# Performance work log

Hardware: AMD Instinct MI355X
Metric: run time of the kernel (lower is better)

The kernel has to match this reference:

```python
import jax, jax.numpy as jnp
import numpy as np

B, L, S, D, H, TOPK = 8, 2048, 1000, 1024, 8, 10
E = D // H  # d_keys = 128


def setup_inputs() -> dict:
    key = jax.random.key(0)
    ks = jax.random.split(key, 8)
    s = 1.0 / np.sqrt(D)
    return {
        "target_embedding": jax.random.normal(ks[0], (B, L, D), dtype=jnp.float32),
        "source_embedding": jax.random.normal(ks[1], (S, D), dtype=jnp.float32),
        "Wq": jax.random.normal(ks[2], (D, D), dtype=jnp.float32) * s,
        "bq": jnp.zeros((D,), dtype=jnp.float32),
        "Wk": jax.random.normal(ks[3], (D, D), dtype=jnp.float32) * s,
        "bk": jnp.zeros((D,), dtype=jnp.float32),
        "Wo": jax.random.normal(ks[4], (D, D), dtype=jnp.float32) * s,
        "bo": jnp.zeros((D,), dtype=jnp.float32),
        "data_id": 0,
    }


def reference(target_embedding, source_embedding, Wq, bq, Wk, bk, Wo, bo, data_id):
    # data_id is unused by the original module's math.
    b, l, d = target_embedding.shape
    h, e, topk = H, E, TOPK
    scale = 1.0 / np.sqrt(e)

    q = (target_embedding @ Wq + bq).reshape(b, l, h, e)   # [B,L,H,E]
    k = (source_embedding @ Wk + bk).reshape(-1, h, e)      # [S,H,E]

    scores = jnp.einsum('blhe,she->bhls', q, k)             # [B,H,L,S]
    A = jax.nn.softmax(scale * scores, axis=-1)             # dropout is eval-mode identity
    tmps = A.sum(axis=2)                                    # [B,H,S] head-wise column mass
    _, idxs = jax.lax.top_k(tmps, topk)                     # [B,H,topk]

    kh = jnp.transpose(k, (1, 0, 2))                        # [H,S,E]
    # gather per (batch, head) the topk source key vectors
    tok = kh[jnp.arange(h)[None, :, None], idxs, :]         # [B,H,topk,E]
    tok = jnp.transpose(tok, (0, 2, 1, 3)).reshape(b, topk, h * e)  # [B,topk,D]
    return tok @ Wo + bo                                    # [B,topk,D]
```

## Files before the change

kernel.cpp:

```cpp
#include <hip/hip_runtime.h>
#include <hip/hip_bf16.h>
#include <math.h>

constexpr int B_ = 8;
constexpr int L_ = 2048;
constexpr int S_ = 1000;
constexpr int D_ = 1024;
constexpr int H_ = 8;
constexpr int E_ = 128;
constexpr int TOPK_ = 10;
constexpr float SCALE_LOG2E_ = 0.12751744f;

typedef __attribute__((ext_vector_type(8))) short short8;
typedef __attribute__((ext_vector_type(4))) float f32x4;

__device__ inline unsigned short f2bf(float x) {
    unsigned u = __float_as_uint(x);
    unsigned r = (u + 0x7fffu + ((u >> 16) & 1u)) >> 16;
    return (unsigned short)r;
}
__device__ inline float bf2f(unsigned short s) {
    return __uint_as_float(((unsigned)s) << 16);
}

__device__ __forceinline__ float fexp2(float x) {
#if __has_builtin(__builtin_amdgcn_exp2f)
    return __builtin_amdgcn_exp2f(x);
#else
    return __expf(x * 0.69314718056f);
#endif
}

typedef __attribute__((address_space(1))) const unsigned int gas_u32;
typedef __attribute__((address_space(3))) unsigned int las_u32;
__device__ __forceinline__ void gload_lds16(const void* g, void* l) {
    __builtin_amdgcn_global_load_lds((gas_u32*)g, (las_u32*)l, 16, 0, 0);
}

__global__ __launch_bounds__(256) void gemm_bias_kernel(
    const float* __restrict__ A, const float* __restrict__ Bm,
    const float* __restrict__ bias, float* __restrict__ C,
    int M, int N, int Kd)
{
    __shared__ float As[16][65];
    __shared__ float Bs[16][68];

    const int t  = threadIdx.x;
    const int tx = t & 15;
    const int ty = t >> 4;
    const int m0 = blockIdx.y * 64;
    const int n0 = blockIdx.x * 64;

    float acc[4][4];
#pragma unroll
    for (int i = 0; i < 4; ++i)
#pragma unroll
        for (int j = 0; j < 4; ++j) acc[i][j] = 0.f;

    for (int k0 = 0; k0 < Kd; k0 += 16) {
        {
            const int row = t >> 2;
            const int c4  = (t & 3) * 4;
            float4 v = {0.f, 0.f, 0.f, 0.f};
            if (m0 + row < M)
                v = *(const float4*)&A[(size_t)(m0 + row) * Kd + k0 + c4];
            As[c4 + 0][row] = v.x;
            As[c4 + 1][row] = v.y;
            As[c4 + 2][row] = v.z;
            As[c4 + 3][row] = v.w;
        }
        {
            const int row = t >> 4;
            const int c4  = (t & 15) * 4;
            float4 v = *(const float4*)&Bm[(size_t)(k0 + row) * N + n0 + c4];
            *(float4*)&Bs[row][c4] = v;
        }
        __syncthreads();
#pragma unroll
        for (int k = 0; k < 16; ++k) {
            float a[4], b[4];
#pragma unroll
            for (int i = 0; i < 4; ++i) a[i] = As[k][ty * 4 + i];
            float4 bv = *(const float4*)&Bs[k][tx * 4];
            b[0] = bv.x; b[1] = bv.y; b[2] = bv.z; b[3] = bv.w;
#pragma unroll
            for (int i = 0; i < 4; ++i)
#pragma unroll
                for (int j = 0; j < 4; ++j) acc[i][j] += a[i] * b[j];
        }
        __syncthreads();
    }

#pragma unroll
    for (int i = 0; i < 4; ++i) {
        const int row = m0 + ty * 4 + i;
        if (row < M) {
#pragma unroll
            for (int j = 0; j < 4; ++j) {
                const int col = n0 + tx * 4 + j;
                C[(size_t)row * N + col] = acc[i][j] + bias[col];
            }
        }
    }
}

__global__ __launch_bounds__(256) void splitWT_kernel(
    const float* __restrict__ W,
    unsigned short* __restrict__ WTh, unsigned short* __restrict__ WTl)
{
    __shared__ __attribute__((aligned(16))) float tile[64][68];
    const int t  = threadIdx.x;
    const int k0 = blockIdx.y * 64, n0 = blockIdx.x * 64;
#pragma unroll
    for (int it = 0; it < 4; ++it) {
        int id = it * 256 + t;
        int r = id >> 4, c = id & 15;
        *(float4*)&tile[r][c * 4] = *(const float4*)&W[(size_t)(k0 + r) * D_ + n0 + c * 4];
    }
    __syncthreads();
#pragma unroll
    for (int it = 0; it < 4; ++it) {
        int id = it * 256 + t;
        int n = id >> 4, c = id & 15;
        unsigned short hs[4], ls[4];
#pragma unroll
        for (int i = 0; i < 4; ++i) {
            float x = tile[c * 4 + i][n];
            hs[i] = f2bf(x);
            ls[i] = f2bf(x - bf2f(hs[i]));
        }
        size_t o = (size_t)(n0 + n) * D_ + k0 + c * 4;
        uint2 uh; uh.x = (unsigned)hs[0] | ((unsigned)hs[1] << 16);
                  uh.y = (unsigned)hs[2] | ((unsigned)hs[3] << 16);
        uint2 ul; ul.x = (unsigned)ls[0] | ((unsigned)ls[1] << 16);
                  ul.y = (unsigned)ls[2] | ((unsigned)ls[3] << 16);
        *(uint2*)&WTh[o] = uh;
        *(uint2*)&WTl[o] = ul;
    }
}

__global__ __launch_bounds__(256) void split_src_kernel(
    const float* __restrict__ src,
    unsigned short* __restrict__ Sh, unsigned short* __restrict__ Sl)
{
    int idx  = blockIdx.x * 256 + threadIdx.x;
    int base = idx * 4;
    int row  = base >> 10;
    float4 v = {0.f, 0.f, 0.f, 0.f};
    if (row < S_) v = *(const float4*)&src[base];
    float xs[4] = {v.x, v.y, v.z, v.w};
    unsigned short hs[4], ls[4];
#pragma unroll
    for (int i = 0; i < 4; ++i) {
        hs[i] = f2bf(xs[i]);
        ls[i] = f2bf(xs[i] - bf2f(hs[i]));
    }
    uint2 uh; uh.x = (unsigned)hs[0] | ((unsigned)hs[1] << 16);
              uh.y = (unsigned)hs[2] | ((unsigned)hs[3] << 16);
    uint2 ul; ul.x = (unsigned)ls[0] | ((unsigned)ls[1] << 16);
              ul.y = (unsigned)ls[2] | ((unsigned)ls[3] << 16);
    *(uint2*)&Sh[base] = uh;
    *(uint2*)&Sl[base] = ul;
}

__global__ __launch_bounds__(256, 2) void kproj_kernel(
    const unsigned short* __restrict__ Sh, const unsigned short* __restrict__ Sl,
    const unsigned short* __restrict__ WkTh, const unsigned short* __restrict__ WkTl,
    const float* __restrict__ bk,
    float* __restrict__ Kbuf,
    unsigned short* __restrict__ Kh, unsigned short* __restrict__ Kl)
{
    __shared__ __attribute__((aligned(16))) unsigned short Ah[128 * 64];
    __shared__ __attribute__((aligned(16))) unsigned short Al[128 * 64];
    __shared__ __attribute__((aligned(16))) unsigned short Bh[128 * 64];
    __shared__ __attribute__((aligned(16))) unsigned short Bl[128 * 64];

    const int t    = threadIdx.x;
    const int lane = t & 63, w = t >> 6;
    const int mb   = blockIdx.x >> 3;
    const int n0   = (blockIdx.x & 7) * 128;

    f32x4 acc[2][8];
#pragma unroll
    for (int m = 0; m < 2; ++m)
#pragma unroll
        for (int n = 0; n < 8; ++n) acc[m][n] = (f32x4){0.f, 0.f, 0.f, 0.f};

    for (int k0 = 0; k0 < D_; k0 += 64) {
        __syncthreads();
#pragma unroll
        for (int it = 0; it < 4; ++it) {
            int r = it * 32 + (t >> 3), c = t & 7;
            size_t gofs = (size_t)r * D_ + k0 + ((c ^ (r & 7)) << 3);
            int db = it * 4096 + t * 16;
            gload_lds16(&Sh[(size_t)(mb * 128) * D_ + gofs], (char*)Ah + db);
            gload_lds16(&Sl[(size_t)(mb * 128) * D_ + gofs], (char*)Al + db);
            gload_lds16(&WkTh[(size_t)n0 * D_ + gofs], (char*)Bh + db);
            gload_lds16(&WkTl[(size_t)n0 * D_ + gofs], (char*)Bl + db);
        }
        __syncthreads();

#pragma unroll
        for (int ki = 0; ki < 2; ++ki) {
            short8 ah[2], al[2];
#pragma unroll
            for (int m = 0; m < 2; ++m) {
                int r = w * 32 + m * 16 + (lane & 15);
                int slot = ki * 4 + (lane >> 4);
                int lofs = r * 64 + ((slot ^ (r & 7)) << 3);
                ah[m] = *(short8*)&Ah[lofs];
                al[m] = *(short8*)&Al[lofs];
            }
#pragma unroll
            for (int n = 0; n < 8; ++n) {
                int nn = n * 16 + (lane & 15);
                int slot = ki * 4 + (lane >> 4);
                int lofs = nn * 64 + ((slot ^ (nn & 7)) << 3);
                short8 bh = *(short8*)&Bh[lofs];
                short8 bl = *(short8*)&Bl[lofs];
#pragma unroll
                for (int m = 0; m < 2; ++m) {
                    acc[m][n] = __builtin_amdgcn_mfma_f32_16x16x32_bf16(ah[m], bh, acc[m][n], 0, 0, 0);
                    acc[m][n] = __builtin_amdgcn_mfma_f32_16x16x32_bf16(ah[m], bl, acc[m][n], 0, 0, 0);
                    acc[m][n] = __builtin_amdgcn_mfma_f32_16x16x32_bf16(al[m], bh, acc[m][n], 0, 0, 0);
                }
            }
        }
    }

#pragma unroll
    for (int n = 0; n < 8; ++n) {
        int col = n0 + n * 16 + (lane & 15);
        float bkv = bk[col];
#pragma unroll
        for (int m = 0; m < 2; ++m) {
            int rbase = mb * 128 + w * 32 + m * 16 + ((lane >> 4) << 2);
#pragma unroll
            for (int r = 0; r < 4; ++r) {
                int row = rbase + r;
                unsigned short hh = 0, ll = 0;
                if (row < S_) {
                    float kv = acc[m][n][r] + bkv;
                    Kbuf[(size_t)row * D_ + col] = kv;
                    hh = f2bf(kv);
                    ll = f2bf(kv - bf2f(hh));
                }
                Kh[(size_t)row * D_ + col] = hh;
                Kl[(size_t)row * D_ + col] = ll;
            }
        }
    }
}

__global__ __launch_bounds__(256, 2) void qproj_kernel(
    const float* __restrict__ tgt,
    const unsigned short* __restrict__ WqTh, const unsigned short* __restrict__ WqTl,
    const float* __restrict__ bq,
    unsigned short* __restrict__ qhb, unsigned short* __restrict__ qlb)
{
    __shared__ __attribute__((aligned(16))) unsigned short Ah[128 * 64];
    __shared__ __attribute__((aligned(16))) unsigned short Al[128 * 64];
    __shared__ __attribute__((aligned(16))) unsigned short Bh[128 * 64];
    __shared__ __attribute__((aligned(16))) unsigned short Bl[128 * 64];

    const int t    = threadIdx.x;
    const int lane = t & 63, w = t >> 6;
    const int mb   = blockIdx.x >> 3;
    const int n0   = (blockIdx.x & 7) * 128;

    f32x4 acc[2][8];
#pragma unroll
    for (int m = 0; m < 2; ++m)
#pragma unroll
        for (int n = 0; n < 8; ++n) acc[m][n] = (f32x4){0.f, 0.f, 0.f, 0.f};

    for (int k0 = 0; k0 < D_; k0 += 64) {
        __syncthreads();
#pragma unroll
        for (int it = 0; it < 4; ++it) {
            int r = it * 32 + (t >> 3), c = t & 7;
            size_t gb = (size_t)(n0 + r) * D_ + k0 + ((c ^ (r & 7)) << 3);
            int db = it * 4096 + t * 16;
            gload_lds16(&WqTh[gb], (char*)Bh + db);
            gload_lds16(&WqTl[gb], (char*)Bl + db);
        }
#pragma unroll
        for (int it = 0; it < 4; ++it) {
            int id = it * 256 + t;
            int r = id >> 3, c = id & 7;
            int lofs = r * 64 + ((c ^ (r & 7)) << 3);
            const float* ga = &tgt[(size_t)(mb * 128 + r) * D_ + k0 + c * 8];
            float4 v0 = *(const float4*)ga;
            float4 v1 = *(const float4*)(ga + 4);
            float xs[8] = {v0.x, v0.y, v0.z, v0.w, v1.x, v1.y, v1.z, v1.w};
            unsigned short hs[8], ls[8];
#pragma unroll
            for (int j = 0; j < 8; ++j) {
                __hip_bfloat16 hb = __float2bfloat16(xs[j]);
                hs[j] = *(unsigned short*)&hb;
                __hip_bfloat16 lb = __float2bfloat16(xs[j] - __bfloat162float(hb));
                ls[j] = *(unsigned short*)&lb;
            }
            uint4 uh, ul;
            uh.x = (unsigned)hs[0] | ((unsigned)hs[1] << 16);
            uh.y = (unsigned)hs[2] | ((unsigned)hs[3] << 16);
            uh.z = (unsigned)hs[4] | ((unsigned)hs[5] << 16);
            uh.w = (unsigned)hs[6] | ((unsigned)hs[7] << 16);
            ul.x = (unsigned)ls[0] | ((unsigned)ls[1] << 16);
            ul.y = (unsigned)ls[2] | ((unsigned)ls[3] << 16);
            ul.z = (unsigned)ls[4] | ((unsigned)ls[5] << 16);
            ul.w = (unsigned)ls[6] | ((unsigned)ls[7] << 16);
            *(uint4*)&Ah[lofs] = uh;
            *(uint4*)&Al[lofs] = ul;
        }
        __syncthreads();

#pragma unroll
        for (int ki = 0; ki < 2; ++ki) {
            short8 ah[2], al[2];
#pragma unroll
            for (int m = 0; m < 2; ++m) {
                int r = w * 32 + m * 16 + (lane & 15);
                int slot = ki * 4 + (lane >> 4);
                int lofs = r * 64 + ((slot ^ (r & 7)) << 3);
                ah[m] = *(short8*)&Ah[lofs];
                al[m] = *(short8*)&Al[lofs];
            }
#pragma unroll
            for (int n = 0; n < 8; ++n) {
                int nn = n * 16 + (lane & 15);
                int slot = ki * 4 + (lane >> 4);
                int lofs = nn * 64 + ((slot ^ (nn & 7)) << 3);
                short8 bh = *(short8*)&Bh[lofs];
                short8 bl = *(short8*)&Bl[lofs];
#pragma unroll
                for (int m = 0; m < 2; ++m) {
                    acc[m][n] = __builtin_amdgcn_mfma_f32_16x16x32_bf16(ah[m], bh, acc[m][n], 0, 0, 0);
                    acc[m][n] = __builtin_amdgcn_mfma_f32_16x16x32_bf16(ah[m], bl, acc[m][n], 0, 0, 0);
                    acc[m][n] = __builtin_amdgcn_mfma_f32_16x16x32_bf16(al[m], bh, acc[m][n], 0, 0, 0);
                }
            }
        }
    }

#pragma unroll
    for (int n = 0; n < 8; ++n) {
        int col = n0 + n * 16 + (lane & 15);
        float bqv = bq[col];
#pragma unroll
        for (int m = 0; m < 2; ++m) {
            int rbase = mb * 128 + w * 32 + m * 16 + ((lane >> 4) << 2);
#pragma unroll
            for (int r = 0; r < 4; ++r) {
                float q = (acc[m][n][r] + bqv) * SCALE_LOG2E_;
                unsigned short hh = f2bf(q);
                qhb[(size_t)(rbase + r) * D_ + col] = hh;
                qlb[(size_t)(rbase + r) * D_ + col] = f2bf(q - bf2f(hh));
            }
        }
    }
}

__global__ __launch_bounds__(256, 4) void scores2p_kernel(
    const unsigned short* __restrict__ qhb, const unsigned short* __restrict__ qlb,
    const unsigned short* __restrict__ Kh, const unsigned short* __restrict__ Kl,
    float* __restrict__ tmps, int b0)
{
    __shared__ __attribute__((aligned(16))) unsigned short SH[2][32 * 128];
    __shared__ __attribute__((aligned(16))) unsigned short SL[2][32 * 128];
    __shared__ float tmps_l[1024];

    const int t    = threadIdx.x;
    const int lane = t & 63, w = t >> 6;
    const int blk  = blockIdx.x;
    const int bb   = blk >> 7;
    const int h    = (blk >> 4) & 7;
    const int lt   = blk & 15;
    const int qrow0 = bb * L_ + lt * 128;
    const int bh_i  = (b0 + bb) * H_ + h;
    const int kr0   = t >> 4;
    const int kc0   = t & 15;

    for (int i = t; i < 1024; i += 256) tmps_l[i] = 0.f;

#define SC_ISSUE(ST, BUF)                                                   \
    do {                                                                    \
        _Pragma("unroll")                                                   \
        for (int it = 0; it < 2; ++it) {                                    \
            int r = it * 16 + kr0;                                          \
            size_t g = (size_t)((ST) * 32 + r) * D_ + h * E_                \
                       + ((kc0 ^ (r & 15)) << 3);                           \
            int db = it * 4096 + t * 16;                                    \
            gload_lds16(&Kh[g], (char*)&SH[(BUF)][0] + db);                 \
            gload_lds16(&Kl[g], (char*)&SL[(BUF)][0] + db);                 \
        }                                                                   \
    } while (0)

    SC_ISSUE(0, 1);

    short8 qh[2][4], ql[2][4];
#pragma unroll
    for (int ch = 0; ch < 4; ++ch) {
        __syncthreads();
#pragma unroll
        for (int it = 0; it < 2; ++it) {
            int r = it * 16 + kr0;
            size_t g = (size_t)(qrow0 + ch * 32 + r) * D_ + h * E_ + kc0 * 8;
            int lofs = r * 128 + ((kc0 ^ (r & 15)) << 3);
            *(uint4*)&SH[0][lofs] = *(const uint4*)&qhb[g];
            *(uint4*)&SL[0][lofs] = *(const uint4*)&qlb[g];
        }
        __syncthreads();
        if (w == ch) {
#pragma unroll
            for (int rg = 0; rg < 2; ++rg)
#pragma unroll
                for (int ki = 0; ki < 4; ++ki) {
                    int rq = rg * 16 + (lane & 15);
                    int slot = ki * 4 + (lane >> 4);
                    int lofs = rq * 128 + ((slot ^ (rq & 15)) << 3);
                    qh[rg][ki] = *(short8*)&SH[0][lofs];
                    ql[rg][ki] = *(short8*)&SL[0][lofs];
                }
        }
    }

    float zacc[2][4];
#pragma unroll
    for (int rg = 0; rg < 2; ++rg)
#pragma unroll
        for (int r = 0; r < 4; ++r) zacc[rg][r] = 0.f;
    float invZ[2][4];

    int cur = 1;
    for (int u = 0; u < 64; ++u) {
        const int st = u & 31;
        __syncthreads();
        if (u < 63) SC_ISSUE((u + 1) & 31, cur ^ 1);

        f32x4 acc[2][2];
#pragma unroll
        for (int rg = 0; rg < 2; ++rg)
#pragma unroll
            for (int nf = 0; nf < 2; ++nf) acc[rg][nf] = (f32x4){0.f, 0.f, 0.f, 0.f};

#pragma unroll
        for (int ki = 0; ki < 4; ++ki)
#pragma unroll
            for (int nf = 0; nf < 2; ++nf) {
                int sr = nf * 16 + (lane & 15);
                int slot = ki * 4 + (lane >> 4);
                int lofs = sr * 128 + ((slot ^ (sr & 15)) << 3);
                short8 bh = *(short8*)&SH[cur][lofs];
                short8 bl = *(short8*)&SL[cur][lofs];
#pragma unroll
                for (int rg = 0; rg < 2; ++rg) {
                    acc[rg][nf] = __builtin_amdgcn_mfma_f32_16x16x32_bf16(qh[rg][ki], bh, acc[rg][nf], 0, 0, 0);
                    acc[rg][nf] = __builtin_amdgcn_mfma_f32_16x16x32_bf16(qh[rg][ki], bl, acc[rg][nf], 0, 0, 0);
                    acc[rg][nf] = __builtin_amdgcn_mfma_f32_16x16x32_bf16(ql[rg][ki], bh, acc[rg][nf], 0, 0, 0);
                }
            }

        if (u < 32) {
#pragma unroll
            for (int nf = 0; nf < 2; ++nf) {
                int s = st * 32 + nf * 16 + (lane & 15);
                if (s < S_) {
#pragma unroll
                    for (int rg = 0; rg < 2; ++rg)
#pragma unroll
                        for (int r = 0; r < 4; ++r)
                            zacc[rg][r] += fexp2(acc[rg][nf][r]);
                }
            }
            if (u == 31) {
#pragma unroll
                for (int rg = 0; rg < 2; ++rg)
#pragma unroll
                    for (int r = 0; r < 4; ++r) {
                        float z = zacc[rg][r];
                        z += __shfl_xor(z, 1);
                        z += __shfl_xor(z, 2);
                        z += __shfl_xor(z, 4);
                        z += __shfl_xor(z, 8);
                        invZ[rg][r] = 1.f / z;
                    }
            }
        } else {
#pragma unroll
            for (int nf = 0; nf < 2; ++nf) {
                int s = st * 32 + nf * 16 + (lane & 15);
                if (s < S_) {
                    float val = 0.f;
#pragma unroll
                    for (int rg = 0; rg < 2; ++rg)
#pragma unroll
                        for (int r = 0; r < 4; ++r)
                            val += fexp2(acc[rg][nf][r]) * invZ[rg][r];
                    atomicAdd(&tmps_l[s], val);
                }
            }
        }
        cur ^= 1;
    }
#undef SC_ISSUE

    __syncthreads();
    for (int i = t; i < S_; i += 256)
        atomicAdd(&tmps[(size_t)bh_i * S_ + i], tmps_l[i]);
}

__global__ __launch_bounds__(256) void topk_kernel(
    const float* __restrict__ tmps, int* __restrict__ idxs)
{
    const int bh = blockIdx.x;
    const int t  = threadIdx.x;
    __shared__ float v[S_];
    __shared__ float rv[256];
    __shared__ int   ri[256];

    for (int i = t; i < S_; i += 256) v[i] = tmps[(size_t)bh * S_ + i];
    __syncthreads();

    for (int it = 0; it < TOPK_; ++it) {
        float best = -1e38f;
        int bi = 0x7fffffff;
        for (int s = t; s < S_; s += 256) {
            const float x = v[s];
            if (x > best) { best = x; bi = s; }
        }
        rv[t] = best; ri[t] = bi;
        __syncthreads();
        for (int k = 128; k > 0; k >>= 1) {
            if (t < k) {
                const float x = rv[t + k];
                const int  xi = ri[t + k];
                if (x > rv[t] || (x == rv[t] && xi < ri[t])) { rv[t] = x; ri[t] = xi; }
            }
            __syncthreads();
        }
        if (t == 0) {
            idxs[bh * TOPK_ + it] = ri[0];
            v[ri[0]] = -1e38f;
        }
        __syncthreads();
    }
}

__global__ __launch_bounds__(256) void gather_kernel(
    const float* __restrict__ K, const int* __restrict__ idxs,
    float* __restrict__ tok)
{
    const int o = blockIdx.x * 256 + threadIdx.x;
    if (o >= B_ * TOPK_ * D_) return;
    const int d  = o & (D_ - 1);
    const int tt = (o >> 10) % TOPK_;
    const int b  = o / (D_ * TOPK_);
    const int h  = d >> 7;
    const int s  = idxs[(b * H_ + h) * TOPK_ + tt];
    tok[o] = K[(size_t)s * D_ + d];
}

extern "C" void kernel_launch(void* const* d_in, const int* in_sizes, int n_in,
                              void* d_out, int out_size, void* d_ws, size_t ws_size,
                              hipStream_t stream)
{
    const float* tgt = (const float*)d_in[0];
    const float* src = (const float*)d_in[1];
    const float* Wq  = (const float*)d_in[2];
    const float* bq  = (const float*)d_in[3];
    const float* Wk  = (const float*)d_in[4];
    const float* bk  = (const float*)d_in[5];
    const float* Wo  = (const float*)d_in[6];
    const float* bo  = (const float*)d_in[7];
    float* out = (float*)d_out;

    char* ws = (char*)d_ws;
    size_t off = 0;
    float*          Kbuf = (float*)(ws + off);          off += (size_t)S_ * D_ * 4;
    float*          tmps = (float*)(ws + off);          off += (size_t)B_ * H_ * S_ * 4;
    int*            idxs = (int*)(ws + off);            off += (size_t)B_ * H_ * TOPK_ * 4;
    off = (off + 255) & ~(size_t)255;
    float*          tok  = (float*)(ws + off);          off += (size_t)B_ * TOPK_ * D_ * 4;
    unsigned short* Kh   = (unsigned short*)(ws + off); off += (size_t)1024 * D_ * 2;
    unsigned short* Kl   = (unsigned short*)(ws + off); off += (size_t)1024 * D_ * 2;
    unsigned short* WqTh = (unsigned short*)(ws + off); off += (size_t)D_ * D_ * 2;
    unsigned short* WqTl = (unsigned short*)(ws + off); off += (size_t)D_ * D_ * 2;
    unsigned short* WkTh = (unsigned short*)(ws + off); off += (size_t)D_ * D_ * 2;
    unsigned short* WkTl = (unsigned short*)(ws + off); off += (size_t)D_ * D_ * 2;
    unsigned short* Sh   = (unsigned short*)(ws + off); off += (size_t)1024 * D_ * 2;
    unsigned short* Sl   = (unsigned short*)(ws + off); off += (size_t)1024 * D_ * 2;
    unsigned short* qhb  = (unsigned short*)(ws + off);
    const size_t fixed_bytes = off;
    const size_t q_plane_b = (size_t)L_ * D_ * 2;

    int nb_fit = 1;
    if (ws_size > fixed_bytes) {
        size_t f = (ws_size - fixed_bytes) / (2 * q_plane_b);
        nb_fit = (f < 1) ? 1 : (f > 8 ? 8 : (int)f);
    }

    hipMemsetAsync(tmps, 0, (size_t)B_ * H_ * S_ * sizeof(float), stream);

    split_src_kernel<<<(1024 * D_) / (256 * 4), 256, 0, stream>>>(src, Sh, Sl);
    {
        dim3 g(D_ / 64, D_ / 64);
        splitWT_kernel<<<g, 256, 0, stream>>>(Wq, WqTh, WqTl);
        splitWT_kernel<<<g, 256, 0, stream>>>(Wk, WkTh, WkTl);
    }

    kproj_kernel<<<64, 256, 0, stream>>>(Sh, Sl, WkTh, WkTl, bk, Kbuf, Kh, Kl);

    for (int b0 = 0; b0 < B_; b0 += nb_fit) {
        int nb = (B_ - b0 < nb_fit) ? (B_ - b0) : nb_fit;
        unsigned short* qlb = qhb + (size_t)nb_fit * q_plane_b / 2;
        qproj_kernel<<<nb * 128, 256, 0, stream>>>(
            tgt + (size_t)b0 * L_ * D_, WqTh, WqTl, bq, qhb, qlb);
        scores2p_kernel<<<nb * 128, 256, 0, stream>>>(qhb, qlb, Kh, Kl, tmps, b0);
    }

    topk_kernel<<<B_ * H_, 256, 0, stream>>>(tmps, idxs);
    gather_kernel<<<(B_ * TOPK_ * D_ + 255) / 256, 256, 0, stream>>>(Kbuf, idxs, tok);
    {
        dim3 g(D_ / 64, (B_ * TOPK_ + 63) / 64);
        gemm_bias_kernel<<<g, 256, 0, stream>>>(tok, Wo, bo, out, B_ * TOPK_, D_, D_);
    }
}
```

Before: 447.7 us.

## Pre-split target to bf16 planes, double-buffer qproj, split score passes

A separate kernel now splits the target embeddings into hi/lo bf16 planes, so qproj can load both operands asynchronously straight into LDS. qproj becomes a double-buffered pipeline with 32-wide K tiles instead of a synchronous 64-wide load-convert loop. The scores kernel is restructured into two loops: the first pass (normalizer) loads only the hi K plane, and the second pass computes column mass. This costs an extra full write and read of the target planes in global memory and halves the batch chunk that fits in the workspace.

```diff
diff --git a/kernel.cpp b/kernel.cpp
--- a/kernel.cpp
+++ b/kernel.cpp
@@ -163,6 +163,28 @@
     *(uint2*)&Sl[base] = ul;
 }
 
+__global__ __launch_bounds__(256) void split_tgt_kernel(
+    const float* __restrict__ tgt,
+    unsigned short* __restrict__ Th, unsigned short* __restrict__ Tl)
+{
+    int idx  = blockIdx.x * 256 + threadIdx.x;
+    int base = idx * 4;
+    float4 v = *(const float4*)&tgt[base];
+    float xs[4] = {v.x, v.y, v.z, v.w};
+    unsigned short hs[4], ls[4];
+#pragma unroll
+    for (int i = 0; i < 4; ++i) {
+        hs[i] = f2bf(xs[i]);
+        ls[i] = f2bf(xs[i] - bf2f(hs[i]));
+    }
+    uint2 uh; uh.x = (unsigned)hs[0] | ((unsigned)hs[1] << 16);
+              uh.y = (unsigned)hs[2] | ((unsigned)hs[3] << 16);
+    uint2 ul; ul.x = (unsigned)ls[0] | ((unsigned)ls[1] << 16);
+              ul.y = (unsigned)ls[2] | ((unsigned)ls[3] << 16);
+    *(uint2*)&Th[base] = uh;
+    *(uint2*)&Tl[base] = ul;
+}
+
 __global__ __launch_bounds__(256, 2) void kproj_kernel(
     const unsigned short* __restrict__ Sh, const unsigned short* __restrict__ Sl,
     const unsigned short* __restrict__ WkTh, const unsigned short* __restrict__ WkTl,
@@ -253,15 +275,15 @@
 }
 
 __global__ __launch_bounds__(256, 2) void qproj_kernel(
-    const float* __restrict__ tgt,
+    const unsigned short* __restrict__ Th, const unsigned short* __restrict__ Tl,
     const unsigned short* __restrict__ WqTh, const unsigned short* __restrict__ WqTl,
     const float* __restrict__ bq,
     unsigned short* __restrict__ qhb, unsigned short* __restrict__ qlb)
 {
-    __shared__ __attribute__((aligned(16))) unsigned short Ah[128 * 64];
-    __shared__ __attribute__((aligned(16))) unsigned short Al[128 * 64];
-    __shared__ __attribute__((aligned(16))) unsigned short Bh[128 * 64];
-    __shared__ __attribute__((aligned(16))) unsigned short Bl[128 * 64];
+    __shared__ __attribute__((aligned(16))) unsigned short Ah[2][128 * 32];
+    __shared__ __attribute__((aligned(16))) unsigned short Al[2][128 * 32];
+    __shared__ __attribute__((aligned(16))) unsigned short Bh[2][128 * 32];
+    __shared__ __attribute__((aligned(16))) unsigned short Bl[2][128 * 32];
 
     const int t    = threadIdx.x;
     const int lane = t & 63, w = t >> 6;
@@ -274,74 +296,51 @@
 #pragma unroll
         for (int n = 0; n < 8; ++n) acc[m][n] = (f32x4){0.f, 0.f, 0.f, 0.f};
 
-    for (int k0 = 0; k0 < D_; k0 += 64) {
-        __syncthreads();
-#pragma unroll
-        for (int it = 0; it < 4; ++it) {
-            int r = it * 32 + (t >> 3), c = t & 7;
-            size_t gb = (size_t)(n0 + r) * D_ + k0 + ((c ^ (r & 7)) << 3);
-            int db = it * 4096 + t * 16;
-            gload_lds16(&WqTh[gb], (char*)Bh + db);
-            gload_lds16(&WqTl[gb], (char*)Bl + db);
-        }
-#pragma unroll
-        for (int it = 0; it < 4; ++it) {
-            int id = it * 256 + t;
-            int r = id >> 3, c = id & 7;
-            int lofs = r * 64 + ((c ^ (r & 7)) << 3);
-            const float* ga = &tgt[(size_t)(mb * 128 + r) * D_ + k0 + c * 8];
-            float4 v0 = *(const float4*)ga;
-            float4 v1 = *(const float4*)(ga + 4);
-            float xs[8] = {v0.x, v0.y, v0.z, v0.w, v1.x, v1.y, v1.z, v1.w};
-            unsigned short hs[8], ls[8];
-#pragma unroll
-            for (int j = 0; j < 8; ++j) {
-                __hip_bfloat16 hb = __float2bfloat16(xs[j]);
-                hs[j] = *(unsigned short*)&hb;
-                __hip_bfloat16 lb = __float2bfloat16(xs[j] - __bfloat162float(hb));
-                ls[j] = *(unsigned short*)&lb;
-            }
-            uint4 uh, ul;
-            uh.x = (unsigned)hs[0] | ((unsigned)hs[1] << 16);
-            uh.y = (unsigned)hs[2] | ((unsigned)hs[3] << 16);
-            uh.z = (unsigned)hs[4] | ((unsigned)hs[5] << 16);
-            uh.w = (unsigned)hs[6] | ((unsigned)hs[7] << 16);
-            ul.x = (unsigned)ls[0] | ((unsigned)ls[1] << 16);
-            ul.y = (unsigned)ls[2] | ((unsigned)ls[3] << 16);
-            ul.z = (unsigned)ls[4] | ((unsigned)ls[5] << 16);
-            ul.w = (unsigned)ls[6] | ((unsigned)ls[7] << 16);
-            *(uint4*)&Ah[lofs] = uh;
-            *(uint4*)&Al[lofs] = ul;
-        }
-        __syncthreads();
-
-#pragma unroll
-        for (int ki = 0; ki < 2; ++ki) {
-            short8 ah[2], al[2];
+#define QP_ISSUE(KT, BUF)                                                   \
+    do {                                                                    \
+        _Pragma("unroll")                                                   \
+        for (int it = 0; it < 2; ++it) {                                    \
+            int id = it * 256 + t;                                          \
+            int r = id >> 2, c = id & 3;                                    \
+            size_t gofs = (size_t)r * D_ + (KT) * 32 + ((c ^ (r & 3)) << 3);\
+            int db = it * 4096 + t * 16;                                    \
+            gload_lds16(&Th[(size_t)(mb * 128) * D_ + gofs], (char*)&Ah[(BUF)][0] + db); \
+            gload_lds16(&Tl[(size_t)(mb * 128) * D_ + gofs], (char*)&Al[(BUF)][0] + db); \
+            gload_lds16(&WqTh[(size_t)n0 * D_ + gofs], (char*)&Bh[(BUF)][0] + db); \
+            gload_lds16(&WqTl[(size_t)n0 * D_ + gofs], (char*)&Bl[(BUF)][0] + db); \
+        }                                                                   \
+    } while (0)
+
+    QP_ISSUE(0, 0);
+    int cur = 0;
+    for (int kt = 0; kt < 32; ++kt) {
+        __syncthreads();
+        if (kt < 31) QP_ISSUE(kt + 1, cur ^ 1);
+
+        short8 ah[2], al[2];
+#pragma unroll
+        for (int m = 0; m < 2; ++m) {
+            int r = w * 32 + m * 16 + (lane & 15);
+            int lofs = r * 32 + ((((lane >> 4)) ^ (r & 3)) << 3);
+            ah[m] = *(short8*)&Ah[cur][lofs];
+            al[m] = *(short8*)&Al[cur][lofs];
+        }
+#pragma unroll
+        for (int n = 0; n < 8; ++n) {
+            int nn = n * 16 + (lane & 15);
+            int lofs = nn * 32 + ((((lane >> 4)) ^ (nn & 3)) << 3);
+            short8 bh = *(short8*)&Bh[cur][lofs];
+            short8 bl = *(short8*)&Bl[cur][lofs];
 #pragma unroll
             for (int m = 0; m < 2; ++m) {
-                int r = w * 32 + m * 16 + (lane & 15);
-                int slot = ki * 4 + (lane >> 4);
-                int lofs = r * 64 + ((slot ^ (r & 7)) << 3);
-                ah[m] = *(short8*)&Ah[lofs];
-                al[m] = *(short8*)&Al[lofs];
-            }
-#pragma unroll
-            for (int n = 0; n < 8; ++n) {
-                int nn = n * 16 + (lane & 15);
-                int slot = ki * 4 + (lane >> 4);
-                int lofs = nn * 64 + ((slot ^ (nn & 7)) << 3);
-                short8 bh = *(short8*)&Bh[lofs];
-                short8 bl = *(short8*)&Bl[lofs];
-#pragma unroll
-                for (int m = 0; m < 2; ++m) {
-                    acc[m][n] = __builtin_amdgcn_mfma_f32_16x16x32_bf16(ah[m], bh, acc[m][n], 0, 0, 0);
-                    acc[m][n] = __builtin_amdgcn_mfma_f32_16x16x32_bf16(ah[m], bl, acc[m][n], 0, 0, 0);
-                    acc[m][n] = __builtin_amdgcn_mfma_f32_16x16x32_bf16(al[m], bh, acc[m][n], 0, 0, 0);
-                }
-            }
-        }
-    }
+                acc[m][n] = __builtin_amdgcn_mfma_f32_16x16x32_bf16(ah[m], bh, acc[m][n], 0, 0, 0);
+                acc[m][n] = __builtin_amdgcn_mfma_f32_16x16x32_bf16(ah[m], bl, acc[m][n], 0, 0, 0);
+                acc[m][n] = __builtin_amdgcn_mfma_f32_16x16x32_bf16(al[m], bh, acc[m][n], 0, 0, 0);
+            }
+        }
+        cur ^= 1;
+    }
+#undef QP_ISSUE
 
 #pragma unroll
     for (int n = 0; n < 8; ++n) {
@@ -383,7 +382,19 @@
 
     for (int i = t; i < 1024; i += 256) tmps_l[i] = 0.f;
 
-#define SC_ISSUE(ST, BUF)                                                   \
+#define SC_ISSUE1(ST, BUF)                                                  \
+    do {                                                                    \
+        _Pragma("unroll")                                                   \
+        for (int it = 0; it < 2; ++it) {                                    \
+            int r = it * 16 + kr0;                                          \
+            size_t g = (size_t)((ST) * 32 + r) * D_ + h * E_                \
+                       + ((kc0 ^ (r & 15)) << 3);                           \
+            int db = it * 4096 + t * 16;                                    \
+            gload_lds16(&Kh[g], (char*)&SH[(BUF)][0] + db);                 \
+        }                                                                   \
+    } while (0)
+
+#define SC_ISSUE2(ST, BUF)                                                  \
     do {                                                                    \
         _Pragma("unroll")                                                   \
         for (int it = 0; it < 2; ++it) {                                    \
@@ -396,7 +407,7 @@
         }                                                                   \
     } while (0)
 
-    SC_ISSUE(0, 1);
+    SC_ISSUE1(0, 1);
 
     short8 qh[2][4], ql[2][4];
 #pragma unroll
@@ -433,10 +444,60 @@
     float invZ[2][4];
 
     int cur = 1;
-    for (int u = 0; u < 64; ++u) {
-        const int st = u & 31;
-        __syncthreads();
-        if (u < 63) SC_ISSUE((u + 1) & 31, cur ^ 1);
+
+    for (int u = 0; u < 32; ++u) {
+        __syncthreads();
+        if (u < 31) SC_ISSUE1(u + 1, cur ^ 1);
+        else        SC_ISSUE2(0, cur ^ 1);
+
+        f32x4 acc[2][2];
+#pragma unroll
+        for (int rg = 0; rg < 2; ++rg)
+#pragma unroll
+            for (int nf = 0; nf < 2; ++nf) acc[rg][nf] = (f32x4){0.f, 0.f, 0.f, 0.f};
+
+#pragma unroll
+        for (int ki = 0; ki < 4; ++ki)
+#pragma unroll
+            for (int nf = 0; nf < 2; ++nf) {
+                int sr = nf * 16 + (lane & 15);
+                int slot = ki * 4 + (lane >> 4);
+                int lofs = sr * 128 + ((slot ^ (sr & 15)) << 3);
+                short8 bh = *(short8*)&SH[cur][lofs];
+#pragma unroll
+                for (int rg = 0; rg < 2; ++rg)
+                    acc[rg][nf] = __builtin_amdgcn_mfma_f32_16x16x32_bf16(qh[rg][ki], bh, acc[rg][nf], 0, 0, 0);
+            }
+
+#pragma unroll
+        for (int nf = 0; nf < 2; ++nf) {
+            int s = u * 32 + nf * 16 + (lane & 15);
+            if (s < S_) {
+#pragma unroll
+                for (int rg = 0; rg < 2; ++rg)
+#pragma unroll
+                    for (int r = 0; r < 4; ++r)
+                        zacc[rg][r] += fexp2(acc[rg][nf][r]);
+            }
+        }
+        cur ^= 1;
+    }
+
+#pragma unroll
+    for (int rg = 0; rg < 2; ++rg)
+#pragma unroll
+        for (int r = 0; r < 4; ++r) {
+            float z = zacc[rg][r];
+            z += __shfl_xor(z, 1);
+            z += __shfl_xor(z, 2);
+            z += __shfl_xor(z, 4);
+            z += __shfl_xor(z, 8);
+            invZ[rg][r] = 1.f / z;
+        }
+
+    for (int u = 0; u < 32; ++u) {
+        __syncthreads();
+        if (u < 31) SC_ISSUE2(u + 1, cur ^ 1);
 
         f32x4 acc[2][2];
 #pragma unroll
@@ -461,49 +522,23 @@
                 }
             }
 
-        if (u < 32) {
-#pragma unroll
-            for (int nf = 0; nf < 2; ++nf) {
-                int s = st * 32 + nf * 16 + (lane & 15);
-                if (s < S_) {
-#pragma unroll
-                    for (int rg = 0; rg < 2; ++rg)
-#pragma unroll
-                        for (int r = 0; r < 4; ++r)
-                            zacc[rg][r] += fexp2(acc[rg][nf][r]);
-                }
-            }
-            if (u == 31) {
+#pragma unroll
+        for (int nf = 0; nf < 2; ++nf) {
+            int s = u * 32 + nf * 16 + (lane & 15);
+            if (s < S_) {
+                float val = 0.f;
 #pragma unroll
                 for (int rg = 0; rg < 2; ++rg)
 #pragma unroll
-                    for (int r = 0; r < 4; ++r) {
-                        float z = zacc[rg][r];
-                        z += __shfl_xor(z, 1);
-                        z += __shfl_xor(z, 2);
-                        z += __shfl_xor(z, 4);
-                        z += __shfl_xor(z, 8);
-                        invZ[rg][r] = 1.f / z;
-                    }
-            }
-        } else {
-#pragma unroll
-            for (int nf = 0; nf < 2; ++nf) {
-                int s = st * 32 + nf * 16 + (lane & 15);
-                if (s < S_) {
-                    float val = 0.f;
-#pragma unroll
-                    for (int rg = 0; rg < 2; ++rg)
-#pragma unroll
-                        for (int r = 0; r < 4; ++r)
-                            val += fexp2(acc[rg][nf][r]) * invZ[rg][r];
-                    atomicAdd(&tmps_l[s], val);
-                }
+                    for (int r = 0; r < 4; ++r)
+                        val += fexp2(acc[rg][nf][r]) * invZ[rg][r];
+                atomicAdd(&tmps_l[s], val);
             }
         }
         cur ^= 1;
     }
-#undef SC_ISSUE
+#undef SC_ISSUE1
+#undef SC_ISSUE2
 
     __syncthreads();
     for (int i = t; i < S_; i += 256)
@@ -590,13 +625,13 @@
     unsigned short* WkTl = (unsigned short*)(ws + off); off += (size_t)D_ * D_ * 2;
     unsigned short* Sh   = (unsigned short*)(ws + off); off += (size_t)1024 * D_ * 2;
     unsigned short* Sl   = (unsigned short*)(ws + off); off += (size_t)1024 * D_ * 2;
-    unsigned short* qhb  = (unsigned short*)(ws + off);
+    unsigned short* planes = (unsigned short*)(ws + off);
     const size_t fixed_bytes = off;
-    const size_t q_plane_b = (size_t)L_ * D_ * 2;
+    const size_t plane_elems_per_b = (size_t)L_ * D_;
 
     int nb_fit = 1;
     if (ws_size > fixed_bytes) {
-        size_t f = (ws_size - fixed_bytes) / (2 * q_plane_b);
+        size_t f = (ws_size - fixed_bytes) / (4 * plane_elems_per_b * 2);
         nb_fit = (f < 1) ? 1 : (f > 8 ? 8 : (int)f);
     }
 
@@ -613,9 +648,14 @@
 
     for (int b0 = 0; b0 < B_; b0 += nb_fit) {
         int nb = (B_ - b0 < nb_fit) ? (B_ - b0) : nb_fit;
-        unsigned short* qlb = qhb + (size_t)nb_fit * q_plane_b / 2;
-        qproj_kernel<<<nb * 128, 256, 0, stream>>>(
-            tgt + (size_t)b0 * L_ * D_, WqTh, WqTl, bq, qhb, qlb);
+        unsigned short* Th  = planes;
+        unsigned short* Tl  = Th  + (size_t)nb_fit * plane_elems_per_b;
+        unsigned short* qhb = Tl  + (size_t)nb_fit * plane_elems_per_b;
+        unsigned short* qlb = qhb + (size_t)nb_fit * plane_elems_per_b;
+
+        split_tgt_kernel<<<(unsigned)((size_t)nb * L_ * D_ / (256 * 4)), 256, 0, stream>>>(
+            tgt + (size_t)b0 * L_ * D_, Th, Tl);
+        qproj_kernel<<<nb * 128, 256, 0, stream>>>(Th, Tl, WqTh, WqTl, bq, qhb, qlb);
         scores2p_kernel<<<nb * 128, 256, 0, stream>>>(qhb, qlb, Kh, Kl, tmps, b0);
     }
 
```

Result: no change. 454.3 us (+1.5%).
